# Optimization experiments

Measured on AMD Instinct MI355X. Metric: run time of the kernel, lower is better.

## Reference

```python
import jax, jax.numpy as jnp
import numpy as np

FLOW_SCALE = 8.0  # typical pixel displacement magnitude


def setup_inputs() -> dict:
    key = jax.random.key(0)
    k1, k2, k3 = jax.random.split(key, 3)
    tenInput = jax.random.normal(k1, (4, 64, 256, 448), dtype=jnp.float32)
    tenFlow = jax.random.normal(k2, (4, 2, 256, 448), dtype=jnp.float32) * FLOW_SCALE
    tenMetric = jax.random.normal(k3, (4, 1, 256, 448), dtype=jnp.float32)
    return {"tenInput": tenInput, "tenFlow": tenFlow, "tenMetric": tenMetric}


def _softsplat_sum(vals, flow):
    # vals: [C1, H, W] augmented input, flow: [2, H, W] (x-disp, y-disp)
    C1, H, W = vals.shape
    gx = jnp.arange(W, dtype=flow.dtype)
    gy = jnp.arange(H, dtype=flow.dtype)
    fltX = gx[None, :] + flow[0]  # [H, W] target x
    fltY = gy[:, None] + flow[1]  # [H, W] target y
    x0 = jnp.floor(fltX)
    y0 = jnp.floor(fltY)
    x1 = x0 + 1.0
    y1 = y0 + 1.0
    # bilinear splat weights for the 4 neighbors
    wNW = (x1 - fltX) * (y1 - fltY)
    wNE = (fltX - x0) * (y1 - fltY)
    wSW = (x1 - fltX) * (fltY - y0)
    wSE = (fltX - x0) * (fltY - y0)
    valsf = vals.reshape(C1, H * W)
    out = jnp.zeros((C1, H * W), dtype=vals.dtype)
    for xi, yi, w in ((x0, y0, wNW), (x1, y0, wNE), (x0, y1, wSW), (x1, y1, wSE)):
        xi_i = xi.astype(jnp.int32)
        yi_i = yi.astype(jnp.int32)
        valid = (xi_i >= 0) & (xi_i < W) & (yi_i >= 0) & (yi_i < H)
        idx = jnp.where(valid, yi_i * W + xi_i, 0).reshape(-1)   # [H*W]
        wv = jnp.where(valid, w, 0.0).reshape(-1)                # [H*W]
        out = out.at[:, idx].add(valsf * wv[None, :])
    return out.reshape(C1, H, W)


def reference(tenInput, tenFlow, tenMetric):
    # strType == 'softmax': splat [input*exp(metric), exp(metric)], then normalize
    m = jnp.exp(tenMetric)                                 # [B,1,H,W]
    aug = jnp.concatenate([tenInput * m, m], axis=1)       # [B,C+1,H,W]
    out = jax.vmap(_softsplat_sum)(aug, tenFlow)           # [B,C+1,H,W]
    norm = out[:, -1:, :, :]
    norm = jnp.where(norm == 0.0, jnp.ones_like(norm), norm)
    return out[:, :-1, :, :] / norm
```

## Files before the change

### kernel.cpp

```cpp
#include <hip/hip_runtime.h>

constexpr int N = 4;
constexpr int C = 64;
constexpr int H = 256;
constexpr int W = 448;
constexpr int HW = H * W;

constexpr int BSX = 4;
constexpr int BSY = 4;
constexpr int BW_ = W / BSX;
constexpr int BH_ = H / BSY;
constexpr int BINS_PB = BW_ * BH_;
constexpr int BINS = N * BINS_PB;
constexpr int GRPS_PB = BINS_PB / 4;


__device__ __forceinline__ int binsOf(int x0, int y0, int bins[4]) {
    const int x1 = x0 + 1, y1 = y0 + 1;
    int n = 0;
    int bxA = -2, bxB = -2, byA = -2, byB = -2;
    if ((unsigned)x0 < (unsigned)W) bxA = x0 >> 2;
    if ((unsigned)x1 < (unsigned)W) { const int t = x1 >> 2; if (t != bxA) bxB = t; }
    if ((unsigned)y0 < (unsigned)H) byA = y0 >> 2;
    if ((unsigned)y1 < (unsigned)H) { const int t = y1 >> 2; if (t != byA) byB = t; }
    if (byA >= 0) {
        if (bxA >= 0) bins[n++] = byA * BW_ + bxA;
        if (bxB >= 0) bins[n++] = byA * BW_ + bxB;
    }
    if (byB >= 0) {
        if (bxA >= 0) bins[n++] = byB * BW_ + bxA;
        if (bxB >= 0) bins[n++] = byB * BW_ + bxB;
    }
    return n;
}

__global__ __launch_bounds__(1024) void scan_kernel(
    const unsigned* __restrict__ counts,
    unsigned* __restrict__ segstart,
    unsigned capE)
{
    __shared__ unsigned lsum[1024];
    const int tid = threadIdx.x;
    constexpr int VPT = BINS / 1024;
    unsigned v[VPT];
    unsigned s = 0;
#pragma unroll
    for (int i = 0; i < VPT; ++i) { v[i] = counts[tid * VPT + i]; s += v[i]; }
    lsum[tid] = s;
    __syncthreads();
    for (int off = 1; off < 1024; off <<= 1) {
        const unsigned t = (tid >= off) ? lsum[tid - off] : 0u;
        __syncthreads();
        lsum[tid] += t;
        __syncthreads();
    }
    unsigned run = lsum[tid] - s;
#pragma unroll
    for (int i = 0; i < VPT; ++i) {
        segstart[tid * VPT + i] = run < capE ? run : capE;
        run += v[i];
    }
    if (tid == 1023) segstart[BINS] = run < capE ? run : capE;
}

__global__ __launch_bounds__(1024) void fill2_kernel(
    const float* __restrict__ flow,
    const float* __restrict__ metric,
    const unsigned* __restrict__ segstart,
    unsigned* __restrict__ cursor,
    float4* __restrict__ recs,
    unsigned capE)
{
    const int tid = threadIdx.x;
    const int idx = blockIdx.x * 1024 + tid;
    const int b = idx / HW;
    const int p = idx - b * HW;
    const int y = p / W;
    const int x = p - y * W;

    const float fx = (float)x + flow[(b * 2 + 0) * HW + p];
    const float fy = (float)y + flow[(b * 2 + 1) * HW + p];
    const float m  = __expf(metric[b * HW + p]);
    const int x0 = (int)floorf(fx), y0 = (int)floorf(fy);

    int bn[4];
    const int nb = binsOf(x0, y0, bn);
    const float4 rec = make_float4(fx, fy, m, __int_as_float(p));
    const int tb = b * BINS_PB;
    for (int i = 0; i < nb; ++i) {
        const unsigned off = atomicAdd(&cursor[tb + bn[i]], 1u);
        const unsigned slot = segstart[tb + bn[i]] + off;
        if (slot < capE) recs[slot] = rec;
    }
}

__global__ __launch_bounds__(256) void augTC_kernel(
    const float* __restrict__ input,
    const float* __restrict__ flow,
    const float* __restrict__ metric,
    float* __restrict__ aug,
    unsigned* __restrict__ counts)
{
    __shared__ float s_val[128][65];
    __shared__ float s_m[128];

    const int tid = threadIdx.x;
    const int blockPix = blockIdx.x * 128;
    const int b = blockPix / HW;
    const int pb = blockPix - b * HW;

    if (tid < 128) {
        const int p = pb + tid;
        const int y = p / W;
        const int x = p - y * W;
        const float fx = (float)x + flow[(b * 2 + 0) * HW + p];
        const float fy = (float)y + flow[(b * 2 + 1) * HW + p];
        s_m[tid] = __expf(metric[b * HW + p]);

        const int x0 = (int)floorf(fx), y0 = (int)floorf(fy);
        int bn[4];
        const int nb = binsOf(x0, y0, bn);
        const int tb = b * BINS_PB;
        for (int i = 0; i < nb; ++i) atomicAdd(&counts[tb + bn[i]], 1u);
    }

    {
        const int sp = tid & 127;
        const int sc = tid >> 7;
        const float* ib = input + (size_t)b * C * HW + pb + sp;
#pragma unroll
        for (int c = 0; c < 32; ++c) {
            const int ch = 2 * c + sc;
            s_val[sp][ch] = ib[(size_t)ch * HW];
        }
    }
    __syncthreads();

    const int wv = tid >> 6, ln = tid & 63;
    float* abase = aug + ((size_t)b * HW + pb) * 64;
#pragma unroll
    for (int it = 0; it < 32; ++it) {
        const int j = (wv << 5) + it;
        abase[(size_t)j * 64 + ln] = s_val[j][ln] * s_m[j];
    }
}

#define ROW4(J, WGT) do { const float tv_ = v0 * (WGT);                   \
    _Pragma("unroll")                                                     \
    for (int i_ = 0; i_ < 4; ++i_)                                        \
        acc[(J) * 4 + i_] = fmaf(tv_, axx[i_], acc[(J) * 4 + i_]);        \
} while (0)

__global__ __launch_bounds__(256, 2) void gather7(
    const float4* __restrict__ recs,
    const float* __restrict__ aug,
    const unsigned* __restrict__ segstart,
    float* __restrict__ out)
{
    __shared__ float st[4][16][65];
    __shared__ float s_inv[4][16];

    const int tid  = threadIdx.x;
    const int wq   = tid >> 6;
    const int lane = tid & 63;

    const int nwg = gridDim.x;
    const int bid = blockIdx.x;
    const int gg  = (bid & 7) * (nwg >> 3) + (bid >> 3);

    const int b    = gg / GRPS_PB;
    const int rem  = gg - b * GRPS_PB;
    const int by   = rem / (BW_ / 4);
    const int kx   = rem - by * (BW_ / 4);
    const int qy0  = by * BSY;
    const int qx0g = kx * 16;
    const int qx0  = qx0g + wq * BSX;
    const int g    = b * BINS_PB + by * BW_ + kx * 4 + wq;

    const float Xp = (float)(qx0 + (lane & 3));
    const float Yp = (float)(qy0 + ((lane >> 2) & 3));

    float acc[16];
#pragma unroll
    for (int i = 0; i < 16; ++i) acc[i] = 0.0f;
    float nrm = 0.0f;

    const int start = (int)segstart[g];
    const int end   = (int)segstart[g + 1];
    const float* ab = aug + (size_t)b * HW * 64;

    const float4 Z = make_float4(0.0f, 0.0f, 0.0f, __int_as_float(0));
    float4 r0 = Z, r1 = Z, r2 = Z;
    float v0 = 0.0f, v1 = 0.0f;
    if (start + 0 < end) r0 = recs[start + 0];
    if (start + 1 < end) r1 = recs[start + 1];
    if (start + 2 < end) r2 = recs[start + 2];
    if (start + 0 < end) {
        const int p0 = __builtin_amdgcn_readfirstlane(__float_as_int(r0.w));
        v0 = ab[(size_t)p0 * 64 + lane];
    }
    if (start + 1 < end) {
        const int p1 = __builtin_amdgcn_readfirstlane(__float_as_int(r1.w));
        v1 = ab[(size_t)p1 * 64 + lane];
    }

    for (int e = start; e < end; ++e) {
        float4 r3 = Z;
        if (e + 3 < end) r3 = recs[e + 3];
        float v2 = 0.0f;
        if (e + 2 < end) {
            const int p2 = __builtin_amdgcn_readfirstlane(__float_as_int(r2.w));
            v2 = ab[(size_t)p2 * 64 + lane];
        }

        const float fxl = r0.x - (float)qx0;
        const float fyl = r0.y - (float)qy0;
        float axx[4];
#pragma unroll
        for (int i = 0; i < 4; ++i)
            axx[i] = fmaxf(1.0f - fabsf(fxl - (float)i), 0.0f);

        const float fyf = floorf(fyl);
        const int   j0  = (int)fyf;
        const float fr  = fyl - fyf;
        const float wA  = 1.0f - fr, wB = fr;
        switch (j0) {
            case -1: ROW4(0, wB); break;
            case 0:  ROW4(0, wA); ROW4(1, wB); break;
            case 1:  ROW4(1, wA); ROW4(2, wB); break;
            case 2:  ROW4(2, wA); ROW4(3, wB); break;
            default: ROW4(3, wA); break;
        }

        const float axn = fmaxf(1.0f - fabsf(r0.x - Xp), 0.0f);
        const float ayn = fmaxf(1.0f - fabsf(r0.y - Yp), 0.0f);
        nrm = fmaf(r0.z, axn * ayn, nrm);

        r0 = r1; r1 = r2; r2 = r3; v0 = v1; v1 = v2;
    }

    const float inv = (nrm == 0.0f) ? 1.0f : (1.0f / nrm);
#pragma unroll
    for (int px = 0; px < 16; ++px)
        st[wq][px][lane] = acc[px];
    if (lane < 16) s_inv[wq][lane] = inv;
    __syncthreads();

    float* ob = out + (size_t)b * C * HW;
    const int px  = tid & 15;
    const int sub = tid >> 4;
    const int binl = px >> 2;
#pragma unroll
    for (int it = 0; it < 16; ++it) {
        const int k   = it * 16 + sub;
        const int c   = k >> 2;
        const int row = k & 3;
        const int pl  = row * 4 + (px & 3);
        ob[(size_t)c * HW + (qy0 + row) * W + qx0g + px] =
            st[binl][pl][c] * s_inv[binl][pl];
    }
}

__global__ __launch_bounds__(256) void splat_nhwc(
    const float* __restrict__ input,
    const float* __restrict__ flow,
    const float* __restrict__ metric,
    float* __restrict__ scr,
    float* __restrict__ norm)
{
    __shared__ float s_val[128][65];
    __shared__ float s_fx[128], s_fy[128], s_m[128];

    const int tid = threadIdx.x;
    const int nwg = gridDim.x;
    const int bid = blockIdx.x;
    const int swz = (bid & 7) * (nwg >> 3) + (bid >> 3);

    const int blockPix = swz * 128;
    const int b = blockPix / HW;
    const int pb = blockPix - b * HW;

    if (tid < 128) {
        const int p = pb + tid;
        const int y = p / W;
        const int x = p - y * W;
        s_fx[tid] = (float)x + flow[(b * 2 + 0) * HW + p];
        s_fy[tid] = (float)y + flow[(b * 2 + 1) * HW + p];
        s_m[tid]  = __expf(metric[b * HW + p]);
    }
    {
        const int sp = tid & 127;
        const int sc = tid >> 7;
        const float* ib = input + (size_t)b * C * HW + pb + sp;
#pragma unroll
        for (int c = 0; c < 32; ++c) {
            const int ch = 2 * c + sc;
            s_val[sp][ch] = ib[(size_t)ch * HW];
        }
    }
    __syncthreads();

    const int wave = tid >> 6;
    const int lane = tid & 63;
    float* __restrict__ sb = scr + (size_t)b * HW * 64;
    float* __restrict__ nb = norm + b * HW;

    for (int k = 0; k < 32; ++k) {
        const int j = (wave << 5) | k;
        const float fx = s_fx[j], fy = s_fy[j], m = s_m[j];
        const float v = s_val[j][lane] * m;

        const float x0f = floorf(fx), y0f = floorf(fy);
        const int x0 = (int)x0f, y0 = (int)y0f;
        const int x1 = x0 + 1,   y1 = y0 + 1;
        const float wx1 = fx - x0f, wx0 = 1.0f - wx1;
        const float wy1 = fy - y0f, wy0 = 1.0f - wy1;

        const bool vx0 = (x0 >= 0) & (x0 < W);
        const bool vx1 = (x1 >= 0) & (x1 < W);
        const bool vy0 = (y0 >= 0) & (y0 < H);
        const bool vy1 = (y1 >= 0) & (y1 < H);

        if (vx0 & vy0) {
            const float w = wx0 * wy0; const int t = y0 * W + x0;
            atomicAdd(sb + (size_t)t * 64 + lane, v * w);
            if (lane == 0) atomicAdd(nb + t, m * w);
        }
        if (vx1 & vy0) {
            const float w = wx1 * wy0; const int t = y0 * W + x1;
            atomicAdd(sb + (size_t)t * 64 + lane, v * w);
            if (lane == 0) atomicAdd(nb + t, m * w);
        }
        if (vx0 & vy1) {
            const float w = wx0 * wy1; const int t = y1 * W + x0;
            atomicAdd(sb + (size_t)t * 64 + lane, v * w);
            if (lane == 0) atomicAdd(nb + t, m * w);
        }
        if (vx1 & vy1) {
            const float w = wx1 * wy1; const int t = y1 * W + x1;
            atomicAdd(sb + (size_t)t * 64 + lane, v * w);
            if (lane == 0) atomicAdd(nb + t, m * w);
        }
    }
}

__global__ __launch_bounds__(256) void untranspose_norm(
    const float* __restrict__ scr,
    const float* __restrict__ norm,
    float* __restrict__ out)
{
    __shared__ float s_t[64][65];
    __shared__ float s_inv[64];

    const int tid = threadIdx.x;
    const int strips = HW / 64;
    const int b = blockIdx.x / strips;
    const int pblk = (blockIdx.x - b * strips) * 64;

    if (tid < 64) {
        float n = norm[b * HW + pblk + tid];
        s_inv[tid] = (n == 0.0f) ? 1.0f : (1.0f / n);
    }
    const float* sb = scr + ((size_t)b * HW + pblk) * 64;
#pragma unroll
    for (int r = 0; r < 16; ++r) {
        const int pr = r * 4 + (tid >> 6);
        const int c  = tid & 63;
        s_t[pr][c] = sb[(size_t)pr * 64 + c];
    }
    __syncthreads();

    float* ob = out + (size_t)b * C * HW + pblk;
#pragma unroll
    for (int r = 0; r < 16; ++r) {
        const int c   = r * 4 + (tid >> 6);
        const int pix = tid & 63;
        ob[(size_t)c * HW + pix] = s_t[pix][c] * s_inv[pix];
    }
}

__global__ void splat_kernel(const float* __restrict__ input,
                             const float* __restrict__ flow,
                             const float* __restrict__ metric,
                             float* __restrict__ out,
                             float* __restrict__ norm)
{
    int idx = blockIdx.x * blockDim.x + threadIdx.x;
    if (idx >= N * HW) return;
    int b = idx / HW;
    int p = idx - b * HW;
    int y = p / W;
    int x = p - y * W;

    float fx = (float)x + flow[(b * 2 + 0) * HW + p];
    float fy = (float)y + flow[(b * 2 + 1) * HW + p];
    float m  = __expf(metric[b * HW + p]);

    float x0f = floorf(fx), y0f = floorf(fy);
    int x0 = (int)x0f, y0 = (int)y0f;
    int x1 = x0 + 1,   y1 = y0 + 1;
    float wx1 = fx - x0f, wx0 = 1.0f - wx1;
    float wy1 = fy - y0f, wy0 = 1.0f - wy1;

    bool vx0 = (x0 >= 0) & (x0 < W);
    bool vx1 = (x1 >= 0) & (x1 < W);
    bool vy0 = (y0 >= 0) & (y0 < H);
    bool vy1 = (y1 >= 0) & (y1 < H);

    bool vNW = vx0 & vy0, vNE = vx1 & vy0, vSW = vx0 & vy1, vSE = vx1 & vy1;
    float wNW = wx0 * wy0, wNE = wx1 * wy0, wSW = wx0 * wy1, wSE = wx1 * wy1;
    int iNW = y0 * W + x0, iNE = y0 * W + x1, iSW = y1 * W + x0, iSE = y1 * W + x1;

    {
        float* nb = norm + b * HW;
        if (vNW) atomicAdd(nb + iNW, m * wNW);
        if (vNE) atomicAdd(nb + iNE, m * wNE);
        if (vSW) atomicAdd(nb + iSW, m * wSW);
        if (vSE) atomicAdd(nb + iSE, m * wSE);
    }

    const float* ib = input + (size_t)b * C * HW + p;
    float* ob = out + (size_t)b * C * HW;
#pragma unroll 4
    for (int c = 0; c < C; ++c) {
        float v = ib[(size_t)c * HW] * m;
        float* oc = ob + (size_t)c * HW;
        if (vNW) atomicAdd(oc + iNW, v * wNW);
        if (vNE) atomicAdd(oc + iNE, v * wNE);
        if (vSW) atomicAdd(oc + iSW, v * wSW);
        if (vSE) atomicAdd(oc + iSE, v * wSE);
    }
}

__global__ void norm_kernel(float* __restrict__ out,
                            const float* __restrict__ norm)
{
    int idx = blockIdx.x * blockDim.x + threadIdx.x;
    int total = N * C * HW / 4;
    if (idx >= total) return;

    int pixq = idx % (HW / 4);
    int bc   = idx / (HW / 4);
    int b    = bc / C;

    const float4* np4 = (const float4*)(norm + (size_t)b * HW);
    float4 n = np4[pixq];
    n.x = (n.x == 0.0f) ? 1.0f : n.x;
    n.y = (n.y == 0.0f) ? 1.0f : n.y;
    n.z = (n.z == 0.0f) ? 1.0f : n.z;
    n.w = (n.w == 0.0f) ? 1.0f : n.w;

    float4* o4 = (float4*)out;
    float4 v = o4[idx];
    v.x /= n.x; v.y /= n.y; v.z /= n.z; v.w /= n.w;
    o4[idx] = v;
}

extern "C" void kernel_launch(void* const* d_in, const int* in_sizes, int n_in,
                              void* d_out, int out_size, void* d_ws, size_t ws_size,
                              hipStream_t stream)
{
    const float* input  = (const float*)d_in[0];
    const float* flow   = (const float*)d_in[1];
    const float* metric = (const float*)d_in[2];
    float* out = (float*)d_out;

    const size_t augBytes  = (size_t)N * HW * 64 * sizeof(float);
    const size_t metaBytes = ((size_t)BINS * 2 + BINS + 1) * sizeof(unsigned);

    const size_t capFull = (size_t)4 * N * HW;
    const size_t cap2x   = (size_t)2 * N * HW;

    auto need = [&](size_t capE) {
        return augBytes + capE * sizeof(float4) + metaBytes;
    };
    const size_t need_mid = augBytes + (size_t)N * HW * sizeof(float);

    size_t capE = 0;
    if      (ws_size >= need(capFull)) capE = capFull;
    else if (ws_size >= need(cap2x))   capE = cap2x;

    if (capE) {
        float*    aug      = (float*)d_ws;
        float4*   recs     = (float4*)((char*)d_ws + augBytes);
        unsigned* counts   = (unsigned*)(recs + capE);
        unsigned* cursor   = counts + BINS;
        unsigned* segstart = cursor + BINS;

        hipMemsetAsync(counts, 0, 2 * BINS * sizeof(unsigned), stream);
        augTC_kernel<<<N * HW / 128, 256, 0, stream>>>(input, flow, metric,
                                                       aug, counts);
        scan_kernel<<<1, 1024, 0, stream>>>(counts, segstart, (unsigned)capE);
        fill2_kernel<<<N * HW / 1024, 1024, 0, stream>>>(flow, metric, segstart,
                                                         cursor, recs, (unsigned)capE);
        gather7<<<BINS / 4, 256, 0, stream>>>(recs, aug, segstart, out);
    } else if (ws_size >= need_mid) {
        float* scr  = (float*)d_ws;
        float* norm = scr + (size_t)N * HW * 64;
        hipMemsetAsync(scr, 0, need_mid, stream);

        splat_nhwc<<<N * HW / 128, 256, 0, stream>>>(input, flow, metric, scr, norm);
        untranspose_norm<<<N * (HW / 64), 256, 0, stream>>>(scr, norm, out);
    } else {
        float* norm = (float*)d_ws;
        hipMemsetAsync(out,  0, (size_t)N * C * HW * sizeof(float), stream);
        hipMemsetAsync(norm, 0, (size_t)N * HW * sizeof(float), stream);

        splat_kernel<<<(N * HW + 255) / 256, 256, 0, stream>>>(input, flow, metric, out, norm);
        int total = N * C * HW / 4;
        norm_kernel<<<(total + 255) / 256, 256, 0, stream>>>(out, norm);
    }
}
```

Baseline: 363.4 us.

## Use wave-shuffle scan, float4 aug transpose, and branchless gather prefetch

The single-block scan now uses wavefront shuffle prefix sums plus a small 16-entry wave-sum pass, replacing the shared-memory Hillis-Steele loop with its many barriers. The augTC transpose kernel reads input and writes aug with float4 vector accesses instead of scalar ones. The gather kernel's software prefetch drops the per-iteration bounds branches by clamping indices to the last record, and unrolls the loop by two. Together these cut instruction and barrier overhead across three pipeline stages. The trade-off is a few redundant clamped loads at segment ends and possible shared-memory bank conflicts in the transposed float4 accesses.

```diff
diff --git a/kernel.cpp b/kernel.cpp
--- a/kernel.cpp
+++ b/kernel.cpp
@@ -39,22 +39,32 @@
     unsigned* __restrict__ segstart,
     unsigned capE)
 {
-    __shared__ unsigned lsum[1024];
+    __shared__ unsigned wsum[16];
     const int tid = threadIdx.x;
+    const int wv  = tid >> 6;
+    const int ln  = tid & 63;
     constexpr int VPT = BINS / 1024;
     unsigned v[VPT];
     unsigned s = 0;
 #pragma unroll
     for (int i = 0; i < VPT; ++i) { v[i] = counts[tid * VPT + i]; s += v[i]; }
-    lsum[tid] = s;
+
+    unsigned incl = s;
+#pragma unroll
+    for (int off = 1; off < 64; off <<= 1) {
+        const unsigned t = __shfl_up(incl, off);
+        if (ln >= off) incl += t;
+    }
+    if (ln == 63) wsum[wv] = incl;
     __syncthreads();
-    for (int off = 1; off < 1024; off <<= 1) {
-        const unsigned t = (tid >= off) ? lsum[tid - off] : 0u;
-        __syncthreads();
-        lsum[tid] += t;
-        __syncthreads();
-    }
-    unsigned run = lsum[tid] - s;
+    if (tid == 0) {
+        unsigned run = 0;
+#pragma unroll
+        for (int i = 0; i < 16; ++i) { const unsigned t = wsum[i]; wsum[i] = run; run += t; }
+    }
+    __syncthreads();
+
+    unsigned run = wsum[wv] + (incl - s);
 #pragma unroll
     for (int i = 0; i < VPT; ++i) {
         segstart[tid * VPT + i] = run < capE ? run : capE;
@@ -125,23 +135,38 @@
     }
 
     {
-        const int sp = tid & 127;
-        const int sc = tid >> 7;
-        const float* ib = input + (size_t)b * C * HW + pb + sp;
-#pragma unroll
-        for (int c = 0; c < 32; ++c) {
-            const int ch = 2 * c + sc;
-            s_val[sp][ch] = ib[(size_t)ch * HW];
+        const int pq = 4 * (tid & 31);
+        const int cs = tid >> 5;
+        const float* ib = input + (size_t)b * C * HW + pb + pq;
+#pragma unroll
+        for (int it = 0; it < 8; ++it) {
+            const int ch = 8 * it + cs;
+            const float4 f = *(const float4*)&ib[(size_t)ch * HW];
+            s_val[pq + 0][ch] = f.x;
+            s_val[pq + 1][ch] = f.y;
+            s_val[pq + 2][ch] = f.z;
+            s_val[pq + 3][ch] = f.w;
         }
     }
     __syncthreads();
 
-    const int wv = tid >> 6, ln = tid & 63;
-    float* abase = aug + ((size_t)b * HW + pb) * 64;
-#pragma unroll
-    for (int it = 0; it < 32; ++it) {
-        const int j = (wv << 5) + it;
-        abase[(size_t)j * 64 + ln] = s_val[j][ln] * s_m[j];
+    {
+        const int wv  = tid >> 6;
+        const int ln  = tid & 63;
+        const int pxo = ln >> 4;
+        const int cb  = 4 * (ln & 15);
+        float* abase = aug + ((size_t)b * HW + pb) * 64;
+#pragma unroll
+        for (int it = 0; it < 8; ++it) {
+            const int px = wv * 32 + it * 4 + pxo;
+            const float mm = s_m[px];
+            float4 v;
+            v.x = s_val[px][cb + 0] * mm;
+            v.y = s_val[px][cb + 1] * mm;
+            v.z = s_val[px][cb + 2] * mm;
+            v.w = s_val[px][cb + 3] * mm;
+            *(float4*)&abase[(size_t)px * 64 + cb] = v;
+        }
     }
 }
 
@@ -151,7 +176,7 @@
         acc[(J) * 4 + i_] = fmaf(tv_, axx[i_], acc[(J) * 4 + i_]);        \
 } while (0)
 
-__global__ __launch_bounds__(256, 2) void gather7(
+__global__ __launch_bounds__(256, 2) void gather8(
     const float4* __restrict__ recs,
     const float* __restrict__ aug,
     const unsigned* __restrict__ segstart,
@@ -189,54 +214,47 @@
     const int end   = (int)segstart[g + 1];
     const float* ab = aug + (size_t)b * HW * 64;
 
-    const float4 Z = make_float4(0.0f, 0.0f, 0.0f, __int_as_float(0));
-    float4 r0 = Z, r1 = Z, r2 = Z;
-    float v0 = 0.0f, v1 = 0.0f;
-    if (start + 0 < end) r0 = recs[start + 0];
-    if (start + 1 < end) r1 = recs[start + 1];
-    if (start + 2 < end) r2 = recs[start + 2];
-    if (start + 0 < end) {
+    if (start < end) {
+        const int last = end - 1;
+        float4 r0 = recs[start];
+        float4 r1 = recs[min(start + 1, last)];
+        float4 r2 = recs[min(start + 2, last)];
         const int p0 = __builtin_amdgcn_readfirstlane(__float_as_int(r0.w));
-        v0 = ab[(size_t)p0 * 64 + lane];
-    }
-    if (start + 1 < end) {
+        float v0 = ab[(size_t)p0 * 64 + lane];
         const int p1 = __builtin_amdgcn_readfirstlane(__float_as_int(r1.w));
-        v1 = ab[(size_t)p1 * 64 + lane];
-    }
-
-    for (int e = start; e < end; ++e) {
-        float4 r3 = Z;
-        if (e + 3 < end) r3 = recs[e + 3];
-        float v2 = 0.0f;
-        if (e + 2 < end) {
+        float v1 = ab[(size_t)p1 * 64 + lane];
+
+#pragma unroll 2
+        for (int e = start; e < end; ++e) {
+            const float4 r3 = recs[min(e + 3, last)];
             const int p2 = __builtin_amdgcn_readfirstlane(__float_as_int(r2.w));
-            v2 = ab[(size_t)p2 * 64 + lane];
-        }
-
-        const float fxl = r0.x - (float)qx0;
-        const float fyl = r0.y - (float)qy0;
-        float axx[4];
-#pragma unroll
-        for (int i = 0; i < 4; ++i)
-            axx[i] = fmaxf(1.0f - fabsf(fxl - (float)i), 0.0f);
-
-        const float fyf = floorf(fyl);
-        const int   j0  = (int)fyf;
-        const float fr  = fyl - fyf;
-        const float wA  = 1.0f - fr, wB = fr;
-        switch (j0) {
-            case -1: ROW4(0, wB); break;
-            case 0:  ROW4(0, wA); ROW4(1, wB); break;
-            case 1:  ROW4(1, wA); ROW4(2, wB); break;
-            case 2:  ROW4(2, wA); ROW4(3, wB); break;
-            default: ROW4(3, wA); break;
-        }
-
-        const float axn = fmaxf(1.0f - fabsf(r0.x - Xp), 0.0f);
-        const float ayn = fmaxf(1.0f - fabsf(r0.y - Yp), 0.0f);
-        nrm = fmaf(r0.z, axn * ayn, nrm);
-
-        r0 = r1; r1 = r2; r2 = r3; v0 = v1; v1 = v2;
+            const float v2 = ab[(size_t)p2 * 64 + lane];
+
+            const float fxl = r0.x - (float)qx0;
+            const float fyl = r0.y - (float)qy0;
+            float axx[4];
+#pragma unroll
+            for (int i = 0; i < 4; ++i)
+                axx[i] = fmaxf(1.0f - fabsf(fxl - (float)i), 0.0f);
+
+            const float fyf = floorf(fyl);
+            const int   j0  = (int)fyf;
+            const float fr  = fyl - fyf;
+            const float wA  = 1.0f - fr, wB = fr;
+            switch (j0) {
+                case -1: ROW4(0, wB); break;
+                case 0:  ROW4(0, wA); ROW4(1, wB); break;
+                case 1:  ROW4(1, wA); ROW4(2, wB); break;
+                case 2:  ROW4(2, wA); ROW4(3, wB); break;
+                default: ROW4(3, wA); break;
+            }
+
+            const float axn = fmaxf(1.0f - fabsf(r0.x - Xp), 0.0f);
+            const float ayn = fmaxf(1.0f - fabsf(r0.y - Yp), 0.0f);
+            nrm = fmaf(r0.z, axn * ayn, nrm);
+
+            r0 = r1; r1 = r2; r2 = r3; v0 = v1; v1 = v2;
+        }
     }
 
     const float inv = (nrm == 0.0f) ? 1.0f : (1.0f / nrm);
@@ -493,7 +511,7 @@
         scan_kernel<<<1, 1024, 0, stream>>>(counts, segstart, (unsigned)capE);
         fill2_kernel<<<N * HW / 1024, 1024, 0, stream>>>(flow, metric, segstart,
                                                          cursor, recs, (unsigned)capE);
-        gather7<<<BINS / 4, 256, 0, stream>>>(recs, aug, segstart, out);
+        gather8<<<BINS / 4, 256, 0, stream>>>(recs, aug, segstart, out);
     } else if (ws_size >= need_mid) {
         float* scr  = (float*)d_ws;
         float* norm = scr + (size_t)N * HW * 64;
```

New measurement: 356.2 us. 1.02x faster.
